# Kernel optimization log

Hardware: AMD Instinct MI355X
Metric: run time of the kernel (lower is better)

Reference implementation:

```python
import jax, jax.numpy as jnp
import numpy as np

N_NODES = 50000
N_EDGES = 800000
IN_CH = 128
OUT_CH = 64


def setup_inputs() -> dict:
    key = jax.random.key(0)
    ks = jax.random.split(key, 8)
    cat = IN_CH + OUT_CH
    scale = 1.0 / np.sqrt(cat)
    return {
        "x": jax.random.normal(ks[0], (N_NODES, IN_CH), dtype=jnp.float32),
        "edge_index": jax.random.randint(ks[1], (2, N_EDGES), 0, N_NODES, dtype=jnp.int64),
        "edge_weight": jax.random.uniform(ks[2], (N_EDGES,), dtype=jnp.float32),
        "hidden_state": jax.random.normal(ks[3], (N_NODES, OUT_CH), dtype=jnp.float32),
        "W_z": jax.random.normal(ks[4], (cat, OUT_CH), dtype=jnp.float32) * scale,
        "b_z": jnp.zeros((OUT_CH,), dtype=jnp.float32),
        "W_r": jax.random.normal(ks[5], (cat, OUT_CH), dtype=jnp.float32) * scale,
        "b_r": jnp.zeros((OUT_CH,), dtype=jnp.float32),
        "W_h": jax.random.normal(ks[6], (cat, OUT_CH), dtype=jnp.float32) * scale,
        "b_h": jnp.zeros((OUT_CH,), dtype=jnp.float32),
    }


def _gcn_norm(row, col, w, num_nodes):
    # PyG GCNConv normalization with self-loops (fill_value=1):
    # norm_e = deg[row]^-1/2 * w_e * deg[col]^-1/2 over loop-augmented edges
    loops = jnp.arange(num_nodes, dtype=row.dtype)
    row = jnp.concatenate([row, loops])
    col = jnp.concatenate([col, loops])
    w = jnp.concatenate([w, jnp.ones((num_nodes,), dtype=w.dtype)])
    deg = jax.ops.segment_sum(w, col, num_segments=num_nodes)
    dinv = jnp.where(deg > 0, jax.lax.rsqrt(deg), 0.0)
    norm = dinv[row] * w * dinv[col]
    return row, col, norm


def _gcn_conv(x_cat, W, b, row, col, norm, num_nodes):
    h = x_cat @ W                                   # (N, out)
    msg = h[row] * norm[:, None]                    # (E+N, out) gather + scale
    out = jax.ops.segment_sum(msg, col, num_segments=num_nodes)
    return out + b


def reference(x, edge_index, edge_weight, hidden_state,
              W_z, b_z, W_r, b_r, W_h, b_h):
    n = x.shape[0]
    row, col, norm = _gcn_norm(edge_index[0], edge_index[1], edge_weight, n)
    xh = jnp.concatenate([x, hidden_state], axis=1)
    z = jax.nn.sigmoid(_gcn_conv(xh, W_z, b_z, row, col, norm, n))
    r = jax.nn.sigmoid(_gcn_conv(xh, W_r, b_r, row, col, norm, n))
    xrh = jnp.concatenate([x, r * hidden_state], axis=1)
    h_cand = jnp.tanh(_gcn_conv(xrh, W_h, b_h, row, col, norm, n))
    return z * hidden_state + (1.0 - z) * h_cand
```

## Files before the change

kernel.cpp:

```cpp
#include <hip/hip_runtime.h>
#include <hip/hip_bf16.h>
#include <cstdint>
#include <cstddef>

#define IN_CH   128
#define OUT_CH  64
#define CAT_CH  192

typedef short bf16x8 __attribute__((ext_vector_type(8)));
typedef float f32x4  __attribute__((ext_vector_type(4)));
typedef float f32x2  __attribute__((ext_vector_type(2)));
typedef unsigned long long u64;
typedef unsigned int u32;

__device__ __forceinline__ float sigmoidf_(float x) { return 1.f / (1.f + __expf(-x)); }

__device__ __forceinline__ unsigned short f2bf(float f) {
    u32 u = __float_as_uint(f);
    u32 r = (u + 0x7fffu + ((u >> 16) & 1u)) >> 16;
    return (unsigned short)r;
}
__device__ __forceinline__ u32 pk2bf(float a, float b) {
    return (u32)f2bf(a) | ((u32)f2bf(b) << 16);
}
__device__ __forceinline__ float bflo(u32 v) { return __uint_as_float(v << 16); }
__device__ __forceinline__ float bfhi(u32 v) { return __uint_as_float(v & 0xffff0000u); }

__device__ __forceinline__ unsigned char f2e4m3(float f) {
    u32 p = __builtin_amdgcn_cvt_pk_fp8_f32(f, f, 0, false);
    return (unsigned char)p;
}
template <bool HI>
__device__ __forceinline__ f32x2 fp8pk(u32 v) {
    return __builtin_amdgcn_cvt_pk_f32_fp8((int)v, HI);
}

__device__ __forceinline__ int load_col(const void* ei, int i, int E, int f) {
    return f ? ((const int*)ei)[E + i] : (int)((const long long*)ei)[E + i];
}
__device__ __forceinline__ int load_row(const void* ei, int i, int E, int f) {
    return f ? ((const int*)ei)[i] : (int)((const long long*)ei)[i];
}

__global__ void prep_kernel(int4* __restrict__ zdst, int n16,
                            const unsigned int* __restrict__ ei, int* __restrict__ flag,
                            const float* __restrict__ Wz, const float* __restrict__ Wr,
                            const float* __restrict__ Wh,
                            unsigned short* __restrict__ Bzrt, unsigned short* __restrict__ Wht,
                            int gZ) {
    int b = blockIdx.x, t = threadIdx.x;
    if (b < gZ) {
        int i = b * 256 + t;
        if (i < n16) zdst[i] = make_int4(0, 0, 0, 0);
    } else if (b == gZ) {
        if (t < 64) {
            unsigned int v = ei[(t << 1) + 1];
            unsigned long long bl = __ballot(v != 0u);
            if (t == 0) *flag = (bl != 0ull) ? 1 : 0;
        }
    } else {
        int i = (b - gZ - 1) * 256 + t;
        if (i < 192 * CAT_CH) {
            int col = i / CAT_CH, k = i % CAT_CH;
            if (col < 128) {
                float v = (col < 64) ? Wz[k * 64 + col] : Wr[k * 64 + (col - 64)];
                Bzrt[col * CAT_CH + k] = f2bf(v);
            } else {
                Wht[(col - 128) * CAT_CH + k] = f2bf(Wh[k * 64 + (col - 128)]);
            }
        }
    }
}

__global__ void hist2_kernel(const void* __restrict__ ei, const float* __restrict__ w,
                             u64* __restrict__ packed8, u32* __restrict__ rank,
                             const int* __restrict__ flag, int E, int N) {
    int i0 = (blockIdx.x * blockDim.x + threadIdx.x) * 2;
    if (i0 >= E) return;
    const u32 shard = blockIdx.x & 7;
    u64* __restrict__ shp = packed8 + (size_t)shard * N;
    int f = *flag;
    u32 rk[2];
#pragma unroll
    for (int k = 0; k < 2; k++) {
        int i = i0 + k;
        if (i < E) {
            int c = load_col(ei, i, E, f);
            u32 wq = __float2uint_rn(w[i] * 1048576.0f);
            u64 old = atomicAdd(&shp[c], (1ull << 32) | (u64)wq);
            rk[k] = (shard << 28) | (u32)(old >> 32);
        }
    }
#pragma unroll
    for (int k = 0; k < 2; k++)
        if (i0 + k < E) rank[i0 + k] = rk[k];
}

__global__ __launch_bounds__(256) void scan1_kernel(const u64* __restrict__ packed8,
                                                    float* __restrict__ dinv,
                                                    u32* __restrict__ shoff,
                                                    int* __restrict__ starts,
                                                    int* __restrict__ bsum, int n) {
    __shared__ int s[256];
    int i = blockIdx.x * 256 + threadIdx.x;
    int v = 0;
    if (i < n) {
        u32 run = 0, wsum = 0;
#pragma unroll
        for (int sh = 0; sh < 8; sh++) {
            u64 p = packed8[(size_t)sh * n + i];
            shoff[(size_t)sh * n + i] = run;
            run  += (u32)(p >> 32);
            wsum += (u32)p;
        }
        float ws = (float)wsum * (1.0f / 1048576.0f);
        dinv[i] = rsqrtf(1.0f + ws);
        v = (int)run;
    }
    s[threadIdx.x] = v;
    __syncthreads();
#pragma unroll
    for (int d = 1; d < 256; d <<= 1) {
        int t = (threadIdx.x >= d) ? s[threadIdx.x - d] : 0;
        __syncthreads();
        s[threadIdx.x] += t;
        __syncthreads();
    }
    if (i < n) starts[i] = s[threadIdx.x] - v;
    if (threadIdx.x == 255) bsum[blockIdx.x] = s[255];
}

__global__ __launch_bounds__(256) void scan2_kernel(int* __restrict__ bsum, int nb) {
    __shared__ int s[256];
    int t = threadIdx.x;
    int v = (t < nb) ? bsum[t] : 0;
    s[t] = v;
    __syncthreads();
#pragma unroll
    for (int d = 1; d < 256; d <<= 1) {
        int u = (t >= d) ? s[t - d] : 0;
        __syncthreads();
        s[t] += u;
        __syncthreads();
    }
    if (t < nb) bsum[t] = s[t] - v;
}

__global__ void scan3_kernel(int* __restrict__ starts, const int* __restrict__ boff,
                             int n, int E) {
    int i = blockIdx.x * blockDim.x + threadIdx.x;
    if (i == 0) starts[n] = E;
    if (i < n) starts[i] += boff[blockIdx.x];
}

__global__ void scatter2_kernel(const void* __restrict__ ei, const float* __restrict__ w,
                                const float* __restrict__ dinv, const int* __restrict__ starts,
                                const u32* __restrict__ shoff, const u32* __restrict__ rank,
                                u64* __restrict__ pairs, const int* __restrict__ flag,
                                int E, int N) {
    int i0 = (blockIdx.x * blockDim.x + threadIdx.x) * 4;
    if (i0 >= E) return;
    int f = *flag;
    int r[4], c[4];
#pragma unroll
    for (int k = 0; k < 4; k++) {
        int i = i0 + k;
        if (i < E) { r[k] = load_row(ei, i, E, f); c[k] = load_col(ei, i, E, f); }
    }
#pragma unroll
    for (int k = 0; k < 4; k++) {
        int i = i0 + k;
        if (i < E) {
            float nm = dinv[r[k]] * w[i] * dinv[c[k]];
            u32 rk = rank[i];
            u32 sh = rk >> 28, rks = rk & 0x0fffffffu;
            int pos = starts[c[k]] + (int)shoff[(size_t)sh * N + c[k]] + (int)rks;
            pairs[pos] = ((u64)__float_as_uint(nm) << 32) | (u32)(r[k] << 7);
        }
    }
}

template <int TN, bool FP8OUT, bool A1F32>
__global__ __launch_bounds__(256) void gemm_bf16_kernel(
    const float* __restrict__ A0, int a0w,
    const void* __restrict__ A1, int a1w,
    const unsigned short* __restrict__ Bt,
    void* __restrict__ Cout, int nrows)
{
    __shared__ unsigned short As[128][48];
    __shared__ unsigned short Bs[TN][200];

    const int t = threadIdx.x, lane = t & 63, wave = t >> 6;
    const int rowBase = blockIdx.x * 128;

    for (int idx = t * 8; idx < TN * CAT_CH; idx += 256 * 8) {
        int col = idx / CAT_CH, k = idx % CAT_CH;
        *(int4*)&Bs[col][k] = *(const int4*)&Bt[idx];
    }

    f32x4 acc[2][TN / 16];
#pragma unroll
    for (int rf = 0; rf < 2; rf++)
#pragma unroll
        for (int cf = 0; cf < TN / 16; cf++) acc[rf][cf] = (f32x4){0.f, 0.f, 0.f, 0.f};

    const int srow = t >> 1, half = t & 1;
    int arow = rowBase + srow;
    if (arow >= nrows) arow = nrows - 1;

    for (int k0 = 0; k0 < CAT_CH; k0 += 32) {
        __syncthreads();
        {
            int kk = k0 + half * 16;
            u32 pk[8];
            if (kk < a0w) {
                const float* src = A0 + (size_t)arow * a0w + kk;
#pragma unroll
                for (int q = 0; q < 4; q++) {
                    float4 v = *(const float4*)(src + q * 4);
                    pk[q * 2]     = pk2bf(v.x, v.y);
                    pk[q * 2 + 1] = pk2bf(v.z, v.w);
                }
            } else if (A1F32) {
                const float* src = (const float*)A1 + (size_t)arow * a1w + (kk - a0w);
#pragma unroll
                for (int q = 0; q < 4; q++) {
                    float4 v = *(const float4*)(src + q * 4);
                    pk[q * 2]     = pk2bf(v.x, v.y);
                    pk[q * 2 + 1] = pk2bf(v.z, v.w);
                }
            } else {
                const unsigned short* src =
                    (const unsigned short*)A1 + (size_t)arow * a1w + (kk - a0w);
                int4 v0 = *(const int4*)src;
                int4 v1 = *(const int4*)(src + 8);
                pk[0] = v0.x; pk[1] = v0.y; pk[2] = v0.z; pk[3] = v0.w;
                pk[4] = v1.x; pk[5] = v1.y; pk[6] = v1.z; pk[7] = v1.w;
            }
            *(int4*)&As[srow][half * 16]     = make_int4(pk[0], pk[1], pk[2], pk[3]);
            *(int4*)&As[srow][half * 16 + 8] = make_int4(pk[4], pk[5], pk[6], pk[7]);
        }
        __syncthreads();

        const int rbase = wave * 32;
        const int koff = (lane >> 4) * 8;
        bf16x8 a0 = *(const bf16x8*)&As[rbase + (lane & 15)][koff];
        bf16x8 a1 = *(const bf16x8*)&As[rbase + 16 + (lane & 15)][koff];
#pragma unroll
        for (int cf = 0; cf < TN / 16; cf++) {
            bf16x8 b = *(const bf16x8*)&Bs[cf * 16 + (lane & 15)][k0 + koff];
            acc[0][cf] = __builtin_amdgcn_mfma_f32_16x16x32_bf16(a0, b, acc[0][cf], 0, 0, 0);
            acc[1][cf] = __builtin_amdgcn_mfma_f32_16x16x32_bf16(a1, b, acc[1][cf], 0, 0, 0);
        }
    }

#pragma unroll
    for (int rf = 0; rf < 2; rf++)
#pragma unroll
        for (int cf = 0; cf < TN / 16; cf++) {
            int row0 = rowBase + wave * 32 + rf * 16 + (lane >> 4) * 4;
            int col  = cf * 16 + (lane & 15);
#pragma unroll
            for (int r = 0; r < 4; r++) {
                int row = row0 + r;
                if (row < nrows) {
                    if (FP8OUT)
                        ((unsigned char*)Cout)[(size_t)row * TN + col] = f2e4m3(acc[rf][cf][r]);
                    else
                        ((unsigned short*)Cout)[(size_t)row * TN + col] = f2bf(acc[rf][cf][r]);
                }
            }
        }
}

__global__ __launch_bounds__(256) void spmm_zr_kernel(
    const unsigned char* __restrict__ H8, const u64* __restrict__ pairs,
    const int* __restrict__ starts, const float* __restrict__ dinv,
    const float* __restrict__ hidden, const float* __restrict__ bz,
    const float* __restrict__ br, float* __restrict__ Z,
    unsigned short* __restrict__ RHb, int N)
{
    int node = (blockIdx.x * 256 + threadIdx.x) >> 6;
    if (node >= N) return;
    const int lane = threadIdx.x & 63;
    const int sub = lane & 31, half = lane >> 5;
    int s = starts[node], e = starts[node + 1];
    float d = dinv[node], d2 = d * d;

    float a0 = 0.f, a1 = 0.f, a2 = 0.f, a3 = 0.f;
    if (half == 0) {
        u32 sv = *(const u32*)&H8[(size_t)node * 128 + sub * 4];
        f32x2 s01 = fp8pk<false>(sv), s23 = fp8pk<true>(sv);
        a0 = s01.x * d2; a1 = s01.y * d2; a2 = s23.x * d2; a3 = s23.y * d2;
    }

    int j = s;
    int full = s + ((e - s) & ~15);
    for (; j < full; j += 16) {
        u32 hv[8]; float nm[8];
#pragma unroll
        for (int k = 0; k < 8; k++) {
            u64 p = pairs[j + k * 2 + half];
            nm[k] = __uint_as_float((u32)(p >> 32));
            hv[k] = *(const u32*)&H8[(size_t)(u32)p + sub * 4];
        }
#pragma unroll
        for (int k = 0; k < 8; k++) {
            f32x2 h01 = fp8pk<false>(hv[k]), h23 = fp8pk<true>(hv[k]);
            a0 = fmaf(h01.x, nm[k], a0); a1 = fmaf(h01.y, nm[k], a1);
            a2 = fmaf(h23.x, nm[k], a2); a3 = fmaf(h23.y, nm[k], a3);
        }
    }
    if (j < e) {
        u32 hv[8]; float nm[8];
#pragma unroll
        for (int k = 0; k < 8; k++) {
            int jj = j + k * 2 + half;
            u64 p = pairs[(jj < e) ? jj : (e - 1)];
            nm[k] = (jj < e) ? __uint_as_float((u32)(p >> 32)) : 0.f;
            hv[k] = *(const u32*)&H8[(size_t)(u32)p + sub * 4];
        }
#pragma unroll
        for (int k = 0; k < 8; k++) {
            f32x2 h01 = fp8pk<false>(hv[k]), h23 = fp8pk<true>(hv[k]);
            a0 = fmaf(h01.x, nm[k], a0); a1 = fmaf(h01.y, nm[k], a1);
            a2 = fmaf(h23.x, nm[k], a2); a3 = fmaf(h23.y, nm[k], a3);
        }
    }

    a0 += __shfl_xor(a0, 32, 64);
    a1 += __shfl_xor(a1, 32, 64);
    a2 += __shfl_xor(a2, 32, 64);
    a3 += __shfl_xor(a3, 32, 64);

    if (half == 0) {
        if (sub < 16) {
            int c = sub * 4;
            float4 b4 = *(const float4*)&bz[c];
            float4 o = { sigmoidf_(a0 + b4.x), sigmoidf_(a1 + b4.y),
                         sigmoidf_(a2 + b4.z), sigmoidf_(a3 + b4.w) };
            *(float4*)&Z[(size_t)node * 64 + c] = o;
        } else {
            int c = (sub - 16) * 4;
            float4 b4 = *(const float4*)&br[c];
            float4 hid = *(const float4*)&hidden[(size_t)node * 64 + c];
            float r0 = sigmoidf_(a0 + b4.x) * hid.x;
            float r1 = sigmoidf_(a1 + b4.y) * hid.y;
            float r2 = sigmoidf_(a2 + b4.z) * hid.z;
            float r3 = sigmoidf_(a3 + b4.w) * hid.w;
            ushort4 o = { f2bf(r0), f2bf(r1), f2bf(r2), f2bf(r3) };
            *(ushort4*)&RHb[(size_t)node * 64 + c] = o;
        }
    }
}

__global__ __launch_bounds__(256) void spmm_h_kernel(
    const unsigned short* __restrict__ H, const u64* __restrict__ pairs,
    const int* __restrict__ starts, const float* __restrict__ dinv,
    const float* __restrict__ hidden, const float* __restrict__ bh,
    const float* __restrict__ Z, float* __restrict__ out, int N)
{
    int node = (blockIdx.x * 256 + threadIdx.x) >> 6;
    if (node >= N) return;
    const int lane = threadIdx.x & 63;
    const int sub = lane & 31, half = lane >> 5;
    const unsigned char* Hb = (const unsigned char*)H;
    int s = starts[node], e = starts[node + 1];
    float d = dinv[node], d2 = d * d;

    float ax = 0.f, ay = 0.f;
    if (half == 0) {
        u32 sv = *(const u32*)&Hb[(size_t)node * 128 + sub * 4];
        ax = bflo(sv) * d2; ay = bfhi(sv) * d2;
    }

    int j = s;
    int full = s + ((e - s) & ~15);
    for (; j < full; j += 16) {
        u32 hv[8]; float nm[8];
#pragma unroll
        for (int k = 0; k < 8; k++) {
            u64 p = pairs[j + k * 2 + half];
            nm[k] = __uint_as_float((u32)(p >> 32));
            hv[k] = *(const u32*)&Hb[(size_t)(u32)p + sub * 4];
        }
#pragma unroll
        for (int k = 0; k < 8; k++) {
            ax = fmaf(bflo(hv[k]), nm[k], ax);
            ay = fmaf(bfhi(hv[k]), nm[k], ay);
        }
    }
    if (j < e) {
        u32 hv[8]; float nm[8];
#pragma unroll
        for (int k = 0; k < 8; k++) {
            int jj = j + k * 2 + half;
            u64 p = pairs[(jj < e) ? jj : (e - 1)];
            nm[k] = (jj < e) ? __uint_as_float((u32)(p >> 32)) : 0.f;
            hv[k] = *(const u32*)&Hb[(size_t)(u32)p + sub * 4];
        }
#pragma unroll
        for (int k = 0; k < 8; k++) {
            ax = fmaf(bflo(hv[k]), nm[k], ax);
            ay = fmaf(bfhi(hv[k]), nm[k], ay);
        }
    }

    ax += __shfl_xor(ax, 32, 64);
    ay += __shfl_xor(ay, 32, 64);

    if (half == 0) {
        int c = sub * 2;
        size_t idx = (size_t)node * 64 + c;
        float2 hid = *(const float2*)&hidden[idx];
        float2 z   = *(const float2*)&Z[idx];
        float hc0 = tanhf(ax + bh[c]);
        float hc1 = tanhf(ay + bh[c + 1]);
        float2 o = { z.x * hid.x + (1.f - z.x) * hc0,
                     z.y * hid.y + (1.f - z.y) * hc1 };
        *(float2*)&out[idx] = o;
    }
}

extern "C" void kernel_launch(void* const* d_in, const int* in_sizes, int n_in,
                              void* d_out, int out_size, void* d_ws, size_t ws_size,
                              hipStream_t stream) {
    const float* x      = (const float*)d_in[0];
    const void*  eidx   = d_in[1];
    const float* ew     = (const float*)d_in[2];
    const float* hidden = (const float*)d_in[3];
    const float* Wz     = (const float*)d_in[4];
    const float* bz     = (const float*)d_in[5];
    const float* Wr     = (const float*)d_in[6];
    const float* br     = (const float*)d_in[7];
    const float* Wh     = (const float*)d_in[8];
    const float* bh     = (const float*)d_in[9];
    float* out = (float*)d_out;

    const int E = in_sizes[2];
    const int N = in_sizes[3] / OUT_CH;

    char* base = (char*)d_ws;
    size_t off = 0;
    auto carve = [&](size_t bytes) -> char* {
        char* p = base + off;
        off = (off + bytes + 255) & ~(size_t)255;
        return p;
    };
    u64*   packed8 = (u64*) carve((size_t)N * 8 * 8);
    u32*   shoff   = (u32*) carve((size_t)N * 8 * 4);
    u32*   rank    = (u32*) carve((size_t)E * 4);
    float* dinv    = (float*)carve((size_t)N * 4);
    int*   starts  = (int*)  carve((size_t)(N + 1) * 4);
    int*   bsum    = (int*)  carve(256 * 4);
    u64*   pairs   = (u64*)  carve((size_t)E * 8);
    unsigned char*  Hzr8 = (unsigned char*)carve((size_t)N * 128);
    unsigned short* RHb  = (unsigned short*)carve((size_t)N * 64 * 2);
    unsigned short* Hhb  = (unsigned short*)carve((size_t)N * 64 * 2);
    float* Z = (float*)carve((size_t)N * 64 * 4);
    unsigned short* Bzrt = (unsigned short*)carve((size_t)128 * CAT_CH * 2);
    unsigned short* Wht  = (unsigned short*)carve((size_t)64 * CAT_CH * 2);
    int* flag = (int*)carve(4);
    if (off > ws_size) return;

    const int B256 = 256;
    const int gE2 = (E + 511) / 512;
    const int gE4 = (E + 1023) / 1024;
    const int gN = (N + B256 - 1) / B256;
    const int gM = (N + 127) / 128;
    const int gW = (N + 3) / 4;
    const int n16 = N * 4;
    const int gZ = (n16 + B256 - 1) / B256;
    const int gP = (192 * CAT_CH + 255) / 256;

    hipLaunchKernelGGL(prep_kernel, dim3(gZ + 1 + gP), dim3(B256), 0, stream,
                       (int4*)packed8, n16, (const unsigned int*)eidx, flag,
                       Wz, Wr, Wh, Bzrt, Wht, gZ);

    hipLaunchKernelGGL(hist2_kernel, dim3(gE2), dim3(B256), 0, stream,
                       eidx, ew, packed8, rank, flag, E, N);

    hipLaunchKernelGGL(scan1_kernel, dim3(gN), dim3(B256), 0, stream,
                       packed8, dinv, shoff, starts, bsum, N);
    hipLaunchKernelGGL(scan2_kernel, dim3(1), dim3(B256), 0, stream, bsum, gN);
    hipLaunchKernelGGL(scan3_kernel, dim3(gN), dim3(B256), 0, stream, starts, bsum, N, E);

    hipLaunchKernelGGL(scatter2_kernel, dim3(gE4), dim3(B256), 0, stream,
                       eidx, ew, dinv, starts, shoff, rank, pairs, flag, E, N);

    hipLaunchKernelGGL((gemm_bf16_kernel<128, true, true>), dim3(gM), dim3(B256), 0, stream,
                       x, 128, (const void*)hidden, 64, Bzrt, (void*)Hzr8, N);

    hipLaunchKernelGGL(spmm_zr_kernel, dim3(gW), dim3(B256), 0, stream,
                       Hzr8, pairs, starts, dinv, hidden, bz, br, Z, RHb, N);

    hipLaunchKernelGGL((gemm_bf16_kernel<64, false, false>), dim3(gM), dim3(B256), 0, stream,
                       x, 128, (const void*)RHb, 64, Wht, (void*)Hhb, N);

    hipLaunchKernelGGL(spmm_h_kernel, dim3(gW), dim3(B256), 0, stream,
                       Hhb, pairs, starts, dinv, hidden, bh, Z, out, N);
}
```

Baseline: 169.9 us.

## Fuse histogram with z/r GEMM and split h-GEMM into x and rh parts

Merges the edge histogram, the z/r projection GEMM and the x-part of the candidate GEMM into one heterogeneous launch whose blocks take roles by index. This lets atomics-bound histogram work overlap with MFMA GEMM work. The candidate GEMM is split: the x·W_h part is computed early into an fp32 buffer, and a later smaller GEMM over only the 64 r*h columns adds to it. The cost is an extra N×64 fp32 buffer write and read, plus a larger shared-memory footprint for histogram blocks in the fused kernel, which may reduce occupancy.

```diff
diff --git a/kernel.cpp b/kernel.cpp
--- a/kernel.cpp
+++ b/kernel.cpp
@@ -72,130 +72,20 @@
     }
 }
 
-__global__ void hist2_kernel(const void* __restrict__ ei, const float* __restrict__ w,
-                             u64* __restrict__ packed8, u32* __restrict__ rank,
-                             const int* __restrict__ flag, int E, int N) {
-    int i0 = (blockIdx.x * blockDim.x + threadIdx.x) * 2;
-    if (i0 >= E) return;
-    const u32 shard = blockIdx.x & 7;
-    u64* __restrict__ shp = packed8 + (size_t)shard * N;
-    int f = *flag;
-    u32 rk[2];
-#pragma unroll
-    for (int k = 0; k < 2; k++) {
-        int i = i0 + k;
-        if (i < E) {
-            int c = load_col(ei, i, E, f);
-            u32 wq = __float2uint_rn(w[i] * 1048576.0f);
-            u64 old = atomicAdd(&shp[c], (1ull << 32) | (u64)wq);
-            rk[k] = (shard << 28) | (u32)(old >> 32);
-        }
-    }
-#pragma unroll
-    for (int k = 0; k < 2; k++)
-        if (i0 + k < E) rank[i0 + k] = rk[k];
-}
-
-__global__ __launch_bounds__(256) void scan1_kernel(const u64* __restrict__ packed8,
-                                                    float* __restrict__ dinv,
-                                                    u32* __restrict__ shoff,
-                                                    int* __restrict__ starts,
-                                                    int* __restrict__ bsum, int n) {
-    __shared__ int s[256];
-    int i = blockIdx.x * 256 + threadIdx.x;
-    int v = 0;
-    if (i < n) {
-        u32 run = 0, wsum = 0;
-#pragma unroll
-        for (int sh = 0; sh < 8; sh++) {
-            u64 p = packed8[(size_t)sh * n + i];
-            shoff[(size_t)sh * n + i] = run;
-            run  += (u32)(p >> 32);
-            wsum += (u32)p;
-        }
-        float ws = (float)wsum * (1.0f / 1048576.0f);
-        dinv[i] = rsqrtf(1.0f + ws);
-        v = (int)run;
-    }
-    s[threadIdx.x] = v;
-    __syncthreads();
-#pragma unroll
-    for (int d = 1; d < 256; d <<= 1) {
-        int t = (threadIdx.x >= d) ? s[threadIdx.x - d] : 0;
-        __syncthreads();
-        s[threadIdx.x] += t;
-        __syncthreads();
-    }
-    if (i < n) starts[i] = s[threadIdx.x] - v;
-    if (threadIdx.x == 255) bsum[blockIdx.x] = s[255];
-}
-
-__global__ __launch_bounds__(256) void scan2_kernel(int* __restrict__ bsum, int nb) {
-    __shared__ int s[256];
-    int t = threadIdx.x;
-    int v = (t < nb) ? bsum[t] : 0;
-    s[t] = v;
-    __syncthreads();
-#pragma unroll
-    for (int d = 1; d < 256; d <<= 1) {
-        int u = (t >= d) ? s[t - d] : 0;
-        __syncthreads();
-        s[t] += u;
-        __syncthreads();
-    }
-    if (t < nb) bsum[t] = s[t] - v;
-}
-
-__global__ void scan3_kernel(int* __restrict__ starts, const int* __restrict__ boff,
-                             int n, int E) {
-    int i = blockIdx.x * blockDim.x + threadIdx.x;
-    if (i == 0) starts[n] = E;
-    if (i < n) starts[i] += boff[blockIdx.x];
-}
-
-__global__ void scatter2_kernel(const void* __restrict__ ei, const float* __restrict__ w,
-                                const float* __restrict__ dinv, const int* __restrict__ starts,
-                                const u32* __restrict__ shoff, const u32* __restrict__ rank,
-                                u64* __restrict__ pairs, const int* __restrict__ flag,
-                                int E, int N) {
-    int i0 = (blockIdx.x * blockDim.x + threadIdx.x) * 4;
-    if (i0 >= E) return;
-    int f = *flag;
-    int r[4], c[4];
-#pragma unroll
-    for (int k = 0; k < 4; k++) {
-        int i = i0 + k;
-        if (i < E) { r[k] = load_row(ei, i, E, f); c[k] = load_col(ei, i, E, f); }
-    }
-#pragma unroll
-    for (int k = 0; k < 4; k++) {
-        int i = i0 + k;
-        if (i < E) {
-            float nm = dinv[r[k]] * w[i] * dinv[c[k]];
-            u32 rk = rank[i];
-            u32 sh = rk >> 28, rks = rk & 0x0fffffffu;
-            int pos = starts[c[k]] + (int)shoff[(size_t)sh * N + c[k]] + (int)rks;
-            pairs[pos] = ((u64)__float_as_uint(nm) << 32) | (u32)(r[k] << 7);
-        }
-    }
-}
-
-template <int TN, bool FP8OUT, bool A1F32>
-__global__ __launch_bounds__(256) void gemm_bf16_kernel(
-    const float* __restrict__ A0, int a0w,
+template <int TN, int OUT, bool A1F32>
+__device__ __forceinline__ void gemm_body(
+    unsigned short* __restrict__ As , unsigned short* __restrict__ Bs ,
+    int blk, const float* __restrict__ A0, int a0w,
     const void* __restrict__ A1, int a1w,
-    const unsigned short* __restrict__ Bt,
-    void* __restrict__ Cout, int nrows)
+    const unsigned short* __restrict__ Bt, int bOff, int K,
+    const float* __restrict__ Cacc, void* __restrict__ Cout, int nrows)
 {
-    __shared__ unsigned short As[128][48];
-    __shared__ unsigned short Bs[TN][200];
-
     const int t = threadIdx.x, lane = t & 63, wave = t >> 6;
-    const int rowBase = blockIdx.x * 128;
-
-    for (int idx = t * 8; idx < TN * CAT_CH; idx += 256 * 8) {
-        int col = idx / CAT_CH, k = idx % CAT_CH;
-        *(int4*)&Bs[col][k] = *(const int4*)&Bt[idx];
+    const int rowBase = blk * 128;
+
+    for (int idx = t * 8; idx < TN * K; idx += 256 * 8) {
+        int col = idx / K, k = idx % K;
+        *(int4*)&Bs[col * 200 + k] = *(const int4*)&Bt[col * CAT_CH + bOff + k];
     }
 
     f32x4 acc[2][TN / 16];
@@ -208,7 +98,7 @@
     int arow = rowBase + srow;
     if (arow >= nrows) arow = nrows - 1;
 
-    for (int k0 = 0; k0 < CAT_CH; k0 += 32) {
+    for (int k0 = 0; k0 < K; k0 += 32) {
         __syncthreads();
         {
             int kk = k0 + half * 16;
@@ -237,18 +127,18 @@
                 pk[0] = v0.x; pk[1] = v0.y; pk[2] = v0.z; pk[3] = v0.w;
                 pk[4] = v1.x; pk[5] = v1.y; pk[6] = v1.z; pk[7] = v1.w;
             }
-            *(int4*)&As[srow][half * 16]     = make_int4(pk[0], pk[1], pk[2], pk[3]);
-            *(int4*)&As[srow][half * 16 + 8] = make_int4(pk[4], pk[5], pk[6], pk[7]);
+            *(int4*)&As[srow * 48 + half * 16]     = make_int4(pk[0], pk[1], pk[2], pk[3]);
+            *(int4*)&As[srow * 48 + half * 16 + 8] = make_int4(pk[4], pk[5], pk[6], pk[7]);
         }
         __syncthreads();
 
         const int rbase = wave * 32;
         const int koff = (lane >> 4) * 8;
-        bf16x8 a0 = *(const bf16x8*)&As[rbase + (lane & 15)][koff];
-        bf16x8 a1 = *(const bf16x8*)&As[rbase + 16 + (lane & 15)][koff];
+        bf16x8 a0 = *(const bf16x8*)&As[(rbase + (lane & 15)) * 48 + koff];
+        bf16x8 a1 = *(const bf16x8*)&As[(rbase + 16 + (lane & 15)) * 48 + koff];
 #pragma unroll
         for (int cf = 0; cf < TN / 16; cf++) {
-            bf16x8 b = *(const bf16x8*)&Bs[cf * 16 + (lane & 15)][k0 + koff];
+            bf16x8 b = *(const bf16x8*)&Bs[(cf * 16 + (lane & 15)) * 200 + k0 + koff];
             acc[0][cf] = __builtin_amdgcn_mfma_f32_16x16x32_bf16(a0, b, acc[0][cf], 0, 0, 0);
             acc[1][cf] = __builtin_amdgcn_mfma_f32_16x16x32_bf16(a1, b, acc[1][cf], 0, 0, 0);
         }
@@ -264,13 +154,156 @@
             for (int r = 0; r < 4; r++) {
                 int row = row0 + r;
                 if (row < nrows) {
-                    if (FP8OUT)
-                        ((unsigned char*)Cout)[(size_t)row * TN + col] = f2e4m3(acc[rf][cf][r]);
+                    float v = acc[rf][cf][r];
+                    if (Cacc) v += Cacc[(size_t)row * TN + col];
+                    if (OUT == 1)
+                        ((unsigned char*)Cout)[(size_t)row * TN + col] = f2e4m3(v);
+                    else if (OUT == 2)
+                        ((float*)Cout)[(size_t)row * TN + col] = v;
                     else
-                        ((unsigned short*)Cout)[(size_t)row * TN + col] = f2bf(acc[rf][cf][r]);
+                        ((unsigned short*)Cout)[(size_t)row * TN + col] = f2bf(v);
                 }
             }
         }
+}
+
+__global__ __launch_bounds__(256) void work1_kernel(
+    const float* __restrict__ x, const float* __restrict__ hidden,
+    const unsigned short* __restrict__ Bzrt, const unsigned short* __restrict__ Wht,
+    unsigned char* __restrict__ Hzr8, float* __restrict__ Hh32,
+    const void* __restrict__ ei, const float* __restrict__ ew,
+    u64* __restrict__ packed8, u32* __restrict__ rank,
+    const int* __restrict__ flag, int E, int N, int gM)
+{
+    __shared__ unsigned short As[128 * 48];
+    __shared__ unsigned short Bs[128 * 200];
+
+    const int blk = blockIdx.x;
+    int role, idx;
+    if (blk < 3 * gM) { role = blk % 3; idx = blk / 3; }
+    else              { role = 2;       idx = gM + (blk - 3 * gM); }
+
+    if (role == 0) {
+        gemm_body<128, 1, true>(As, Bs, idx, x, 128, (const void*)hidden, 64,
+                                Bzrt, 0, 192, nullptr, (void*)Hzr8, N);
+    } else if (role == 1) {
+        gemm_body<64, 2, false>(As, Bs, idx, x, 128, nullptr, 0,
+                                Wht, 0, 128, nullptr, (void*)Hh32, N);
+    } else {
+        int i0 = (idx * 256 + threadIdx.x) * 2;
+        if (i0 >= E) return;
+        const u32 shard = (u32)blk & 7;
+        u64* __restrict__ shp = packed8 + (size_t)shard * N;
+        int f = *flag;
+        u32 rk[2];
+#pragma unroll
+        for (int k = 0; k < 2; k++) {
+            int i = i0 + k;
+            if (i < E) {
+                int c = load_col(ei, i, E, f);
+                u32 wq = __float2uint_rn(ew[i] * 1048576.0f);
+                u64 old = atomicAdd(&shp[c], (1ull << 32) | (u64)wq);
+                rk[k] = (shard << 28) | (u32)(old >> 32);
+            }
+        }
+#pragma unroll
+        for (int k = 0; k < 2; k++)
+            if (i0 + k < E) rank[i0 + k] = rk[k];
+    }
+}
+
+__global__ __launch_bounds__(256) void gemm2b_kernel(
+    const unsigned short* __restrict__ RHb, const unsigned short* __restrict__ Wht,
+    const float* __restrict__ Hh32, unsigned short* __restrict__ Hhb, int N)
+{
+    __shared__ unsigned short As[128 * 48];
+    __shared__ unsigned short Bs[64 * 200];
+    gemm_body<64, 0, false>(As, Bs, blockIdx.x, nullptr, 0, (const void*)RHb, 64,
+                            Wht, 128, 64, Hh32, (void*)Hhb, N);
+}
+
+__global__ __launch_bounds__(256) void scan1_kernel(const u64* __restrict__ packed8,
+                                                    float* __restrict__ dinv,
+                                                    u32* __restrict__ shoff,
+                                                    int* __restrict__ starts,
+                                                    int* __restrict__ bsum, int n) {
+    __shared__ int s[256];
+    int i = blockIdx.x * 256 + threadIdx.x;
+    int v = 0;
+    if (i < n) {
+        u32 run = 0, wsum = 0;
+#pragma unroll
+        for (int sh = 0; sh < 8; sh++) {
+            u64 p = packed8[(size_t)sh * n + i];
+            shoff[(size_t)sh * n + i] = run;
+            run  += (u32)(p >> 32);
+            wsum += (u32)p;
+        }
+        float ws = (float)wsum * (1.0f / 1048576.0f);
+        dinv[i] = rsqrtf(1.0f + ws);
+        v = (int)run;
+    }
+    s[threadIdx.x] = v;
+    __syncthreads();
+#pragma unroll
+    for (int d = 1; d < 256; d <<= 1) {
+        int t = (threadIdx.x >= d) ? s[threadIdx.x - d] : 0;
+        __syncthreads();
+        s[threadIdx.x] += t;
+        __syncthreads();
+    }
+    if (i < n) starts[i] = s[threadIdx.x] - v;
+    if (threadIdx.x == 255) bsum[blockIdx.x] = s[255];
+}
+
+__global__ __launch_bounds__(256) void scan2_kernel(int* __restrict__ bsum, int nb) {
+    __shared__ int s[256];
+    int t = threadIdx.x;
+    int v = (t < nb) ? bsum[t] : 0;
+    s[t] = v;
+    __syncthreads();
+#pragma unroll
+    for (int d = 1; d < 256; d <<= 1) {
+        int u = (t >= d) ? s[t - d] : 0;
+        __syncthreads();
+        s[t] += u;
+        __syncthreads();
+    }
+    if (t < nb) bsum[t] = s[t] - v;
+}
+
+__global__ void scan3_kernel(int* __restrict__ starts, const int* __restrict__ boff,
+                             int n, int E) {
+    int i = blockIdx.x * blockDim.x + threadIdx.x;
+    if (i == 0) starts[n] = E;
+    if (i < n) starts[i] += boff[blockIdx.x];
+}
+
+__global__ void scatter2_kernel(const void* __restrict__ ei, const float* __restrict__ w,
+                                const float* __restrict__ dinv, const int* __restrict__ starts,
+                                const u32* __restrict__ shoff, const u32* __restrict__ rank,
+                                u64* __restrict__ pairs, const int* __restrict__ flag,
+                                int E, int N) {
+    int i0 = (blockIdx.x * blockDim.x + threadIdx.x) * 4;
+    if (i0 >= E) return;
+    int f = *flag;
+    int r[4], c[4];
+#pragma unroll
+    for (int k = 0; k < 4; k++) {
+        int i = i0 + k;
+        if (i < E) { r[k] = load_row(ei, i, E, f); c[k] = load_col(ei, i, E, f); }
+    }
+#pragma unroll
+    for (int k = 0; k < 4; k++) {
+        int i = i0 + k;
+        if (i < E) {
+            float nm = dinv[r[k]] * w[i] * dinv[c[k]];
+            u32 rk = rank[i];
+            u32 sh = rk >> 28, rks = rk & 0x0fffffffu;
+            int pos = starts[c[k]] + (int)shoff[(size_t)sh * N + c[k]] + (int)rks;
+            pairs[pos] = ((u64)__float_as_uint(nm) << 32) | (u32)(r[k] << 7);
+        }
+    }
 }
 
 __global__ __launch_bounds__(256) void spmm_zr_kernel(
@@ -457,7 +490,8 @@
     unsigned char*  Hzr8 = (unsigned char*)carve((size_t)N * 128);
     unsigned short* RHb  = (unsigned short*)carve((size_t)N * 64 * 2);
     unsigned short* Hhb  = (unsigned short*)carve((size_t)N * 64 * 2);
-    float* Z = (float*)carve((size_t)N * 64 * 4);
+    float* Hh32 = (float*)carve((size_t)N * 64 * 4);
+    float* Z    = (float*)carve((size_t)N * 64 * 4);
     unsigned short* Bzrt = (unsigned short*)carve((size_t)128 * CAT_CH * 2);
     unsigned short* Wht  = (unsigned short*)carve((size_t)64 * CAT_CH * 2);
     int* flag = (int*)carve(4);
@@ -477,8 +511,9 @@
                        (int4*)packed8, n16, (const unsigned int*)eidx, flag,
                        Wz, Wr, Wh, Bzrt, Wht, gZ);
 
-    hipLaunchKernelGGL(hist2_kernel, dim3(gE2), dim3(B256), 0, stream,
-                       eidx, ew, packed8, rank, flag, E, N);
+    hipLaunchKernelGGL(work1_kernel, dim3(2 * gM + gE2), dim3(B256), 0, stream,
+                       x, hidden, Bzrt, Wht, Hzr8, Hh32,
+                       eidx, ew, packed8, rank, flag, E, N, gM);
 
     hipLaunchKernelGGL(scan1_kernel, dim3(gN), dim3(B256), 0, stream,
                        packed8, dinv, shoff, starts, bsum, N);
@@ -488,14 +523,11 @@
     hipLaunchKernelGGL(scatter2_kernel, dim3(gE4), dim3(B256), 0, stream,
                        eidx, ew, dinv, starts, shoff, rank, pairs, flag, E, N);
 
-    hipLaunchKernelGGL((gemm_bf16_kernel<128, true, true>), dim3(gM), dim3(B256), 0, stream,
-                       x, 128, (const void*)hidden, 64, Bzrt, (void*)Hzr8, N);
-
     hipLaunchKernelGGL(spmm_zr_kernel, dim3(gW), dim3(B256), 0, stream,
                        Hzr8, pairs, starts, dinv, hidden, bz, br, Z, RHb, N);
 
-    hipLaunchKernelGGL((gemm_bf16_kernel<64, false, false>), dim3(gM), dim3(B256), 0, stream,
-                       x, 128, (const void*)RHb, 64, Wht, (void*)Hhb, N);
+    hipLaunchKernelGGL(gemm2b_kernel, dim3(gM), dim3(B256), 0, stream,
+                       RHb, Wht, Hh32, Hhb, N);
 
     hipLaunchKernelGGL(spmm_h_kernel, dim3(gW), dim3(B256), 0, stream,
                        Hhb, pairs, starts, dinv, hidden, bh, Z, out, N);
```

Result: faster. 165.5 us (-2.6%).
